# Performance work log

Measured on AMD Instinct MI355X. Metric: run time of the kernel, lower is better.

Reference implementation:

```python
import jax, jax.numpy as jnp
import numpy as np

EPS = 1e-5

def setup_inputs() -> dict:
    key = jax.random.key(0)
    ks = jax.random.split(key, 16)
    N, E, F_IN, DIM, C, G = 100000, 3200000, 128, 64, 10, 512
    inp = {}
    inp['x'] = jax.random.normal(ks[0], (N, F_IN), dtype=jnp.float32)
    inp['edge_index'] = jax.random.randint(ks[1], (2, E), 0, N, dtype=jnp.int64)
    inp['batch'] = jnp.sort(jax.random.randint(ks[2], (N,), 0, G, dtype=jnp.int64))
    inp['num_graphs'] = G
    def lin(k, fi, fo):
        s = 1.0 / np.sqrt(fi)
        kw, kb = jax.random.split(k)
        return (jax.random.uniform(kw, (fi, fo), jnp.float32, -s, s),
                jax.random.uniform(kb, (fo,), jnp.float32, -s, s))
    inp['W1'], inp['b1'] = lin(ks[3], F_IN, DIM)
    inp['W2'], inp['b2'] = lin(ks[4], DIM, DIM)
    inp['W3'], inp['b3'] = lin(ks[5], DIM, DIM)
    inp['W4'], inp['b4'] = lin(ks[6], DIM, DIM)
    for i in range(1, 5):
        inp[f'g{i}'] = jnp.ones((DIM,), jnp.float32)
        inp[f'be{i}'] = jnp.zeros((DIM,), jnp.float32)
    inp['fcW'], inp['fcb'] = lin(ks[7], DIM, C)
    return inp

def _bn(x, g, b):
    # training-mode BatchNorm1d: biased batch stats over node axis
    m = jnp.mean(x, axis=0)
    v = jnp.mean(jnp.square(x - m), axis=0)
    return g * (x - m) * jax.lax.rsqrt(v + EPS) + b

def _gcn_conv(x, W, b, row, col, norm, N):
    xl = x @ W                                  # [N, dim] dense transform first
    msg = norm[:, None] * xl[row]               # gather from source nodes
    out = jnp.zeros((N, xl.shape[1]), xl.dtype).at[col].add(msg)  # scatter to targets
    return out + b

def _forward(x, edge_index, batch, num_graphs,
             W1, b1, g1, be1, W2, b2, g2, be2,
             W3, b3, g3, be3, W4, b4, g4, be4, fcW, fcb):
    N = x.shape[0]
    loops = jnp.arange(N, dtype=edge_index.dtype)
    row = jnp.concatenate([edge_index[0], loops])   # sources (with self-loops)
    col = jnp.concatenate([edge_index[1], loops])   # targets
    deg = jnp.zeros((N,), x.dtype).at[col].add(1.0)
    dis = jnp.where(deg > 0, jax.lax.rsqrt(jnp.maximum(deg, 1.0)), 0.0)
    norm = dis[row] * dis[col]                      # symmetric GCN normalization
    h = _bn(jax.nn.relu(_gcn_conv(x, W1, b1, row, col, norm, N)), g1, be1)
    h = _bn(jax.nn.relu(_gcn_conv(h, W2, b2, row, col, norm, N)), g2, be2)
    h = _bn(jax.nn.relu(_gcn_conv(h, W3, b3, row, col, norm, N)), g3, be3)
    h = _bn(jax.nn.relu(_gcn_conv(h, W4, b4, row, col, norm, N)), g4, be4)
    # global mean pool over graphs
    sums = jax.ops.segment_sum(h, batch, num_segments=num_graphs)
    cnts = jax.ops.segment_sum(jnp.ones((N,), h.dtype), batch, num_segments=num_graphs)
    pooled = sums / jnp.maximum(cnts, 1.0)[:, None]
    logits = pooled @ fcW + fcb
    return jax.nn.log_softmax(logits, axis=-1)

def reference(x, edge_index, batch, num_graphs,
              W1, b1, g1, be1, W2, b2, g2, be2,
              W3, b3, g3, be3, W4, b4, g4, be4, fcW, fcb):
    return _forward(x, edge_index, batch, num_graphs,
                    W1, b1, g1, be1, W2, b2, g2, be2,
                    W3, b3, g3, be3, W4, b4, g4, be4, fcW, fcb)
```

## Files before the change

### kernel.cpp

```cpp
#include <hip/hip_runtime.h>
#include <hip/hip_bf16.h>
#include <math.h>

#define DIM 64
#define NBK_MAX 512
#define PCHUNK 4096
typedef _Float16 f16;
typedef unsigned int uint32;

__global__ __launch_bounds__(256) void k_hist(const int* __restrict__ col, int* __restrict__ bkcnt,
                                              int E, int nbk) {
  __shared__ int lc[NBK_MAX];
  int tid = threadIdx.x;
  for (int i = tid; i < nbk; i += 256) lc[i] = 0;
  __syncthreads();
  int b0 = blockIdx.x * PCHUNK;
  int b1 = min(E, b0 + PCHUNK);
  for (int e = b0 + tid; e < b1; e += 256) atomicAdd(&lc[col[e] >> 8], 1);
  __syncthreads();
  for (int i = tid; i < nbk; i += 256) { int c = lc[i]; if (c) atomicAdd(&bkcnt[i], c); }
}

__global__ __launch_bounds__(256) void k_scank(const int* __restrict__ cnt, int* __restrict__ offs,
                                               int* __restrict__ cur, int nbk) {
  __shared__ int ps[256];
  int t = threadIdx.x;
  int per = (nbk + 255) >> 8;
  int b0 = t * per;
  int s = 0;
  for (int i = 0; i < per; ++i) { int idx = b0 + i; if (idx < nbk) s += cnt[idx]; }
  ps[t] = s;
  __syncthreads();
  for (int d = 1; d < 256; d <<= 1) {
    int v = (t >= d) ? ps[t - d] : 0;
    __syncthreads();
    if (t >= d) ps[t] += v;
    __syncthreads();
  }
  int run = ps[t] - s;
  for (int i = 0; i < per; ++i) {
    int idx = b0 + i;
    if (idx < nbk) { offs[idx] = run; cur[idx] = run; run += cnt[idx]; }
  }
  if (t == 255) offs[nbk] = run;
}

__global__ __launch_bounds__(256) void k_part(const int* __restrict__ row, const int* __restrict__ col,
                                              int* __restrict__ bcur, uint32* __restrict__ recs,
                                              int E, int nbk) {
  __shared__ int lc[NBK_MAX];
  __shared__ int gb[NBK_MAX];
  int tid = threadIdx.x;
  for (int i = tid; i < nbk; i += 256) lc[i] = 0;
  __syncthreads();
  int b0 = blockIdx.x * PCHUNK;
  int b1 = min(E, b0 + PCHUNK);
  for (int e = b0 + tid; e < b1; e += 256) atomicAdd(&lc[col[e] >> 8], 1);
  __syncthreads();
  for (int i = tid; i < nbk; i += 256) {
    int c = lc[i];
    if (c) { gb[i] = atomicAdd(&bcur[i], c); lc[i] = 0; }
  }
  __syncthreads();
  for (int e = b0 + tid; e < b1; e += 256) {
    int r = row[e], c = col[e];
    int k = c >> 8;
    int pos = gb[k] + atomicAdd(&lc[k], 1);
    recs[pos] = ((uint32)r << 8) | (uint32)(c & 255);
  }
}

__global__ __launch_bounds__(256) void k_sort2(const uint32* __restrict__ recs, const int* __restrict__ keyoffs,
                                               int* __restrict__ csrs, int* __restrict__ offs,
                                               int* __restrict__ cnt, float* __restrict__ dis, int N) {
  __shared__ int lc[256];
  __shared__ int ps[256];
  __shared__ int pos[256];
  int b = blockIdx.x, tid = threadIdx.x;
  lc[tid] = 0;
  __syncthreads();
  int beg = keyoffs[b], end = keyoffs[b + 1];
  for (int p = beg + tid; p < end; p += 256) atomicAdd(&lc[recs[p] & 255], 1);
  __syncthreads();
  int my = lc[tid];
  ps[tid] = my;
  __syncthreads();
  for (int d = 1; d < 256; d <<= 1) {
    int v = (tid >= d) ? ps[tid - d] : 0;
    __syncthreads();
    if (tid >= d) ps[tid] += v;
    __syncthreads();
  }
  int epf = ps[tid] - my;
  pos[tid] = beg + epf;
  int node = (b << 8) + tid;
  if (node < N) {
    offs[node] = beg + epf;
    cnt[node] = my;
    dis[node] = rsqrtf((float)(my + 1));
  }
  __syncthreads();
  for (int p = beg + tid; p < end; p += 256) {
    uint32 r = recs[p];
    int q = atomicAdd(&pos[r & 255], 1);
    csrs[q] = (int)(r >> 8);
  }
}

__global__ __launch_bounds__(256) void k_gemm_in(const float* __restrict__ x, const float* __restrict__ W,
                                                 const float* __restrict__ dis, f16* __restrict__ xl,
                                                 int N, int FIN) {
  __shared__ float Ws[128 * DIM];
  __shared__ float vbuf[4][128];
  int tid = threadIdx.x;
  for (int i = tid; i < FIN * DIM; i += 256) Ws[i] = W[i];
  __syncthreads();
  int wave = tid >> 6, lane = tid & 63;
  int stride = gridDim.x * 4;
  for (int n = blockIdx.x * 4 + wave; n < N; n += stride) {
    const float* xr = x + (size_t)n * FIN;
    for (int k = lane; k < FIN; k += 64) vbuf[wave][k] = xr[k];
    float acc = 0.f;
#pragma unroll 16
    for (int k = 0; k < FIN; ++k) acc = fmaf(vbuf[wave][k], Ws[k * DIM + lane], acc);
    xl[(size_t)n * DIM + lane] = (f16)(acc * dis[n]);
  }
}

__global__ __launch_bounds__(256) void k_gemm_bn(const float* __restrict__ y, const float* __restrict__ W,
                                                 const float* __restrict__ gam, const float* __restrict__ bet,
                                                 const float* __restrict__ s1, const float* __restrict__ s2,
                                                 const float* __restrict__ dis, f16* __restrict__ xl, int N) {
  __shared__ float Ws[DIM * DIM];
  __shared__ float aL[DIM], cL[DIM];
  __shared__ float vbuf[4][DIM];
  int tid = threadIdx.x;
  for (int i = tid; i < DIM * DIM; i += 256) Ws[i] = W[i];
  if (tid < DIM) {
    float invN = 1.0f / (float)N;
    float m = s1[tid] * invN;
    float var = s2[tid] * invN - m * m;
    float inv = rsqrtf(var + 1e-5f);
    float a = gam[tid] * inv;
    aL[tid] = a;
    cL[tid] = fmaf(-m, a, bet[tid]);
  }
  __syncthreads();
  int wave = tid >> 6, lane = tid & 63;
  int stride = gridDim.x * 4;
  for (int n = blockIdx.x * 4 + wave; n < N; n += stride) {
    vbuf[wave][lane] = fmaf(aL[lane], y[(size_t)n * DIM + lane], cL[lane]);
    float acc = 0.f;
#pragma unroll
    for (int k = 0; k < DIM; ++k) acc = fmaf(vbuf[wave][k], Ws[k * DIM + lane], acc);
    xl[(size_t)n * DIM + lane] = (f16)(acc * dis[n]);
  }
}

__global__ __launch_bounds__(256) void k_agg(const f16* __restrict__ xl, const int* __restrict__ offs,
                                             const int* __restrict__ cnt, const int* __restrict__ src,
                                             const float* __restrict__ dis, const float* __restrict__ bias,
                                             float* __restrict__ y, float* __restrict__ s1,
                                             float* __restrict__ s2, int N) {
  int tid = threadIdx.x;
  int wave = tid >> 6, lane = tid & 63;
  float ls = 0.f, lq = 0.f;
  float b = bias[lane];
  int stride = gridDim.x * 4;
  for (int n = blockIdx.x * 4 + wave; n < N; n += stride) {
    float di = dis[n];
    float acc = (float)xl[((size_t)n << 6) + lane];
    int p = offs[n];
    int end = p + cnt[n];
    for (; p + 7 < end; p += 8) {
      int a0 = src[p],     a1 = src[p + 1], a2 = src[p + 2], a3 = src[p + 3];
      int a4 = src[p + 4], a5 = src[p + 5], a6 = src[p + 6], a7 = src[p + 7];
      float v0 = (float)xl[((size_t)a0 << 6) + lane];
      float v1 = (float)xl[((size_t)a1 << 6) + lane];
      float v2 = (float)xl[((size_t)a2 << 6) + lane];
      float v3 = (float)xl[((size_t)a3 << 6) + lane];
      float v4 = (float)xl[((size_t)a4 << 6) + lane];
      float v5 = (float)xl[((size_t)a5 << 6) + lane];
      float v6 = (float)xl[((size_t)a6 << 6) + lane];
      float v7 = (float)xl[((size_t)a7 << 6) + lane];
      acc += ((v0 + v1) + (v2 + v3)) + ((v4 + v5) + (v6 + v7));
    }
    for (; p < end; ++p) acc += (float)xl[((size_t)src[p] << 6) + lane];
    float yv = fmaxf(fmaf(di, acc, b), 0.f);
    y[((size_t)n << 6) + lane] = yv;
    ls += yv;
    lq = fmaf(yv, yv, lq);
  }
  __shared__ float rbuf[256];
  rbuf[tid] = ls;
  __syncthreads();
  if (tid < 64) atomicAdd(&s1[tid], rbuf[tid] + rbuf[tid + 64] + rbuf[tid + 128] + rbuf[tid + 192]);
  __syncthreads();
  rbuf[tid] = lq;
  __syncthreads();
  if (tid < 64) atomicAdd(&s2[tid], rbuf[tid] + rbuf[tid + 64] + rbuf[tid + 128] + rbuf[tid + 192]);
}

__global__ __launch_bounds__(256) void k_pool(const float* __restrict__ y, const float* __restrict__ gam,
                                              const float* __restrict__ bet, const float* __restrict__ s1,
                                              const float* __restrict__ s2, const int* __restrict__ batch,
                                              float* __restrict__ pooled, float* __restrict__ gcnt,
                                              int N, int chunk) {
  __shared__ float aL[DIM], cL[DIM];
  int tid = threadIdx.x;
  if (tid < DIM) {
    float invN = 1.0f / (float)N;
    float m = s1[tid] * invN;
    float var = s2[tid] * invN - m * m;
    float inv = rsqrtf(var + 1e-5f);
    float a = gam[tid] * inv;
    aL[tid] = a;
    cL[tid] = fmaf(-m, a, bet[tid]);
  }
  __syncthreads();
  int wave = tid >> 6, lane = tid & 63;
  int wid = blockIdx.x * 4 + wave;
  int n0 = wid * chunk;
  int n1 = min(N, n0 + chunk);
  if (n0 >= N) return;
  int cur_g = batch[n0];
  float acc = 0.f;
  int cntn = 0;
  for (int n = n0; n < n1; ++n) {
    int gi = batch[n];
    if (gi != cur_g) {
      atomicAdd(&pooled[(size_t)cur_g * DIM + lane], acc);
      if (lane == 0) atomicAdd(&gcnt[cur_g], (float)cntn);
      cur_g = gi; acc = 0.f; cntn = 0;
    }
    acc += fmaf(aL[lane], y[(size_t)n * DIM + lane], cL[lane]);
    ++cntn;
  }
  atomicAdd(&pooled[(size_t)cur_g * DIM + lane], acc);
  if (lane == 0) atomicAdd(&gcnt[cur_g], (float)cntn);
}

__global__ __launch_bounds__(256) void k_head(const float* __restrict__ pooled, const float* __restrict__ gcnt,
                                              const float* __restrict__ fcW, const float* __restrict__ fcb,
                                              float* __restrict__ out, int G, int C) {
  int g = blockIdx.x * 256 + threadIdx.x;
  if (g >= G) return;
  float z[16];
  for (int c = 0; c < C; ++c) z[c] = fcb[c];
  float inv = 1.f / fmaxf(gcnt[g], 1.f);
  for (int f = 0; f < DIM; ++f) {
    float p = pooled[(size_t)g * DIM + f] * inv;
    for (int c = 0; c < C; ++c) z[c] = fmaf(p, fcW[f * C + c], z[c]);
  }
  float m = -1e30f;
  for (int c = 0; c < C; ++c) m = fmaxf(m, z[c]);
  float s = 0.f;
  for (int c = 0; c < C; ++c) s += expf(z[c] - m);
  float ls = logf(s);
  for (int c = 0; c < C; ++c) out[(size_t)g * C + c] = z[c] - m - ls;
}

extern "C" void kernel_launch(void* const* d_in, const int* in_sizes, int n_in,
                              void* d_out, int out_size, void* d_ws, size_t ws_size,
                              hipStream_t stream) {
  const float* x    = (const float*)d_in[0];
  const int*   ei   = (const int*)d_in[1];
  const int*   batch= (const int*)d_in[2];
  const float* W1 = (const float*)d_in[4];
  const float* b1 = (const float*)d_in[5];
  const float* W2 = (const float*)d_in[6];
  const float* b2 = (const float*)d_in[7];
  const float* W3 = (const float*)d_in[8];
  const float* b3 = (const float*)d_in[9];
  const float* W4 = (const float*)d_in[10];
  const float* b4 = (const float*)d_in[11];
  const float* g1 = (const float*)d_in[12];
  const float* be1= (const float*)d_in[13];
  const float* g2 = (const float*)d_in[14];
  const float* be2= (const float*)d_in[15];
  const float* g3 = (const float*)d_in[16];
  const float* be3= (const float*)d_in[17];
  const float* g4 = (const float*)d_in[18];
  const float* be4= (const float*)d_in[19];
  const float* fcW= (const float*)d_in[20];
  const float* fcb= (const float*)d_in[21];
  float* out = (float*)d_out;

  int N   = in_sizes[2];
  int E   = in_sizes[1] / 2;
  int FIN = in_sizes[4] / DIM;
  int C   = in_sizes[21];
  int G   = out_size / C;

  int nbk = (N + 255) >> 8;

  char* ws = (char*)d_ws;
  size_t off = 0;
  auto alloc = [&](size_t bytes) { size_t o = off; off = (off + bytes + 255) & ~(size_t)255; return o; };
  size_t o_bkc  = alloc((size_t)nbk * 4);
  size_t o_bn   = alloc(4 * 2 * 64 * 4);
  size_t o_pool = alloc((size_t)G * DIM * 4);
  size_t o_gcnt = alloc((size_t)G * 4);
  size_t zero_bytes = off;
  size_t o_ko   = alloc((size_t)(nbk + 1) * 4);
  size_t o_cur  = alloc((size_t)nbk * 4);
  size_t o_offs = alloc((size_t)N * 4);
  size_t o_cnt  = alloc((size_t)N * 4);
  size_t o_dis  = alloc((size_t)N * 4);
  size_t o_recs = alloc((size_t)E * 4);
  size_t o_csr  = alloc((size_t)E * 4);
  size_t o_xl   = alloc((size_t)N * DIM * 2);
  size_t o_y    = alloc((size_t)N * DIM * 4);
  (void)ws_size;

  int*    bkcnt  = (int*)(ws + o_bkc);
  float*  bn     = (float*)(ws + o_bn);
  float*  pooled = (float*)(ws + o_pool);
  float*  gcnt   = (float*)(ws + o_gcnt);
  int*    keyoffs= (int*)(ws + o_ko);
  int*    bcur   = (int*)(ws + o_cur);
  int*    offs   = (int*)(ws + o_offs);
  int*    cnt    = (int*)(ws + o_cnt);
  float*  dis    = (float*)(ws + o_dis);
  uint32* recs   = (uint32*)(ws + o_recs);
  int*    csrs   = (int*)(ws + o_csr);
  f16*    xl     = (f16*)(ws + o_xl);
  float*  y      = (float*)(ws + o_y);

  hipMemsetAsync(d_ws, 0, zero_bytes, stream);

  const int* row  = ei;
  const int* colp = ei + E;
  int pblk = (E + PCHUNK - 1) / PCHUNK;

  k_hist<<<pblk, 256, 0, stream>>>(colp, bkcnt, E, nbk);
  k_scank<<<1, 256, 0, stream>>>(bkcnt, keyoffs, bcur, nbk);
  k_part<<<pblk, 256, 0, stream>>>(row, colp, bcur, recs, E, nbk);
  k_sort2<<<nbk, 256, 0, stream>>>(recs, keyoffs, csrs, offs, cnt, dis, N);

  k_gemm_in<<<1024, 256, 0, stream>>>(x, W1, dis, xl, N, FIN);
  k_agg<<<2048, 256, 0, stream>>>(xl, offs, cnt, csrs, dis, b1, y, bn + 0, bn + 64, N);
  k_gemm_bn<<<2048, 256, 0, stream>>>(y, W2, g1, be1, bn + 0, bn + 64, dis, xl, N);
  k_agg<<<2048, 256, 0, stream>>>(xl, offs, cnt, csrs, dis, b2, y, bn + 128, bn + 192, N);
  k_gemm_bn<<<2048, 256, 0, stream>>>(y, W3, g2, be2, bn + 128, bn + 192, dis, xl, N);
  k_agg<<<2048, 256, 0, stream>>>(xl, offs, cnt, csrs, dis, b3, y, bn + 256, bn + 320, N);
  k_gemm_bn<<<2048, 256, 0, stream>>>(y, W4, g3, be3, bn + 256, bn + 320, dis, xl, N);
  k_agg<<<2048, 256, 0, stream>>>(xl, offs, cnt, csrs, dis, b4, y, bn + 384, bn + 448, N);
  int nwaves = 2048;
  int chunk = (N + nwaves - 1) / nwaves;
  k_pool<<<nwaves / 4, 256, 0, stream>>>(y, g4, be4, bn + 384, bn + 448, batch, pooled, gcnt, N, chunk);
  k_head<<<(G + 255) / 256, 256, 0, stream>>>(pooled, gcnt, fcW, fcb, out, G, C);
}
```

Baseline: 998.4 us.

## Register-resident GEMM weights with readlane broadcast, fold BN into weights, fp16 activations

The GEMM kernels now keep each lane's weight column in registers and broadcast the row values with readlane, which removes the LDS staging and its syncs. The BatchNorm scale is folded into the weights and the shift into a constant bias per column. The intermediate activation y is stored as fp16 instead of fp32, halving its write and read traffic. The aggregation unroll grows to 16 and the 32-bit index math replaces size_t. The trade-offs are high VGPR pressure (128 floats for the first GEMM), lower occupancy, and reduced precision of the stored activations.

```diff
diff --git a/kernel.cpp b/kernel.cpp
--- a/kernel.cpp
+++ b/kernel.cpp
@@ -7,6 +7,10 @@
 #define PCHUNK 4096
 typedef _Float16 f16;
 typedef unsigned int uint32;
+
+__device__ __forceinline__ float bcast(float v, int k) {
+  return __uint_as_float(__builtin_amdgcn_readlane(__float_as_uint(v), k));
+}
 
 __global__ __launch_bounds__(256) void k_hist(const int* __restrict__ col, int* __restrict__ bkcnt,
                                               int E, int nbk) {
@@ -108,36 +112,100 @@
 }
 
 __global__ __launch_bounds__(256) void k_gemm_in(const float* __restrict__ x, const float* __restrict__ W,
-                                                 const float* __restrict__ dis, f16* __restrict__ xl,
-                                                 int N, int FIN) {
-  __shared__ float Ws[128 * DIM];
-  __shared__ float vbuf[4][128];
-  int tid = threadIdx.x;
-  for (int i = tid; i < FIN * DIM; i += 256) Ws[i] = W[i];
-  __syncthreads();
-  int wave = tid >> 6, lane = tid & 63;
+                                                 const float* __restrict__ dis, f16* __restrict__ xl, int N) {
+  int tid = threadIdx.x;
+  int lane = tid & 63, wave = tid >> 6;
+  float w[128];
+#pragma unroll
+  for (int k = 0; k < 128; ++k) w[k] = W[k * DIM + lane];
   int stride = gridDim.x * 4;
   for (int n = blockIdx.x * 4 + wave; n < N; n += stride) {
-    const float* xr = x + (size_t)n * FIN;
-    for (int k = lane; k < FIN; k += 64) vbuf[wave][k] = xr[k];
+    const float* xr = x + (size_t)n * 128;
+    float x0 = xr[lane];
+    float x1 = xr[64 + lane];
     float acc = 0.f;
-#pragma unroll 16
-    for (int k = 0; k < FIN; ++k) acc = fmaf(vbuf[wave][k], Ws[k * DIM + lane], acc);
-    xl[(size_t)n * DIM + lane] = (f16)(acc * dis[n]);
-  }
-}
-
-__global__ __launch_bounds__(256) void k_gemm_bn(const float* __restrict__ y, const float* __restrict__ W,
+#pragma unroll
+    for (int k = 0; k < 64; ++k) acc = fmaf(bcast(x0, k), w[k], acc);
+#pragma unroll
+    for (int k = 0; k < 64; ++k) acc = fmaf(bcast(x1, k), w[64 + k], acc);
+    xl[((uint32)n << 6) | lane] = (f16)(acc * dis[n]);
+  }
+}
+
+__global__ __launch_bounds__(256) void k_gemm_bn(const f16* __restrict__ y16, const float* __restrict__ W,
                                                  const float* __restrict__ gam, const float* __restrict__ bet,
                                                  const float* __restrict__ s1, const float* __restrict__ s2,
-                                                 const float* __restrict__ dis, f16* __restrict__ xl, int N) {
-  __shared__ float Ws[DIM * DIM];
+                                                 const float* __restrict__ dis, f16* __restrict__ xl,
+                                                 int N, float invN) {
+  int tid = threadIdx.x;
+  int lane = tid & 63, wave = tid >> 6;
+  float w[64];
+  float cb = 0.f;
+#pragma unroll
+  for (int k = 0; k < 64; ++k) {
+    float m = s1[k] * invN;
+    float var = s2[k] * invN - m * m;
+    float a = gam[k] * rsqrtf(var + 1e-5f);
+    float c = fmaf(-m, a, bet[k]);
+    float wk = W[k * DIM + lane];
+    w[k] = a * wk;
+    cb = fmaf(c, wk, cb);
+  }
+  int stride = gridDim.x * 4;
+  for (int n = blockIdx.x * 4 + wave; n < N; n += stride) {
+    float yv = (float)y16[((uint32)n << 6) | lane];
+    float acc = cb;
+#pragma unroll
+    for (int k = 0; k < 64; ++k) acc = fmaf(bcast(yv, k), w[k], acc);
+    xl[((uint32)n << 6) | lane] = (f16)(acc * dis[n]);
+  }
+}
+
+__global__ __launch_bounds__(256) void k_agg(const f16* __restrict__ xl, const int* __restrict__ offs,
+                                             const int* __restrict__ cnt, const int* __restrict__ src,
+                                             const float* __restrict__ dis, const float* __restrict__ bias,
+                                             f16* __restrict__ y, float* __restrict__ s1,
+                                             float* __restrict__ s2, int N) {
+  int tid = threadIdx.x;
+  int wave = tid >> 6, lane = tid & 63;
+  float ls = 0.f, lq = 0.f;
+  float b = bias[lane];
+  int stride = gridDim.x * 4;
+  for (int n = blockIdx.x * 4 + wave; n < N; n += stride) {
+    float di = dis[n];
+    float acc = (float)xl[((uint32)n << 6) | lane];
+    int p = offs[n];
+    int end = p + cnt[n];
+    for (; p + 15 < end; p += 16) {
+      float s = 0.f;
+#pragma unroll
+      for (int j = 0; j < 16; ++j) s += (float)xl[((uint32)src[p + j] << 6) | lane];
+      acc += s;
+    }
+    for (; p < end; ++p) acc += (float)xl[((uint32)src[p] << 6) | lane];
+    float yv = fmaxf(fmaf(di, acc, b), 0.f);
+    y[((uint32)n << 6) | lane] = (f16)yv;
+    ls += yv;
+    lq = fmaf(yv, yv, lq);
+  }
+  __shared__ float rbuf[256];
+  rbuf[tid] = ls;
+  __syncthreads();
+  if (tid < 64) atomicAdd(&s1[tid], rbuf[tid] + rbuf[tid + 64] + rbuf[tid + 128] + rbuf[tid + 192]);
+  __syncthreads();
+  rbuf[tid] = lq;
+  __syncthreads();
+  if (tid < 64) atomicAdd(&s2[tid], rbuf[tid] + rbuf[tid + 64] + rbuf[tid + 128] + rbuf[tid + 192]);
+}
+
+__global__ __launch_bounds__(256) void k_pool(const f16* __restrict__ y, const float* __restrict__ gam,
+                                              const float* __restrict__ bet, const float* __restrict__ s1,
+                                              const float* __restrict__ s2, const int* __restrict__ batch,
+                                              float* __restrict__ pooled, float* __restrict__ gcnt,
+                                              int N, int chunk, float invN) {
   __shared__ float aL[DIM], cL[DIM];
-  __shared__ float vbuf[4][DIM];
-  int tid = threadIdx.x;
-  for (int i = tid; i < DIM * DIM; i += 256) Ws[i] = W[i];
+  int tid = threadIdx.x;
   if (tid < DIM) {
-    float invN = 1.0f / (float)N;
     float m = s1[tid] * invN;
     float var = s2[tid] * invN - m * m;
     float inv = rsqrtf(var + 1e-5f);
@@ -147,82 +215,11 @@
   }
   __syncthreads();
   int wave = tid >> 6, lane = tid & 63;
-  int stride = gridDim.x * 4;
-  for (int n = blockIdx.x * 4 + wave; n < N; n += stride) {
-    vbuf[wave][lane] = fmaf(aL[lane], y[(size_t)n * DIM + lane], cL[lane]);
-    float acc = 0.f;
-#pragma unroll
-    for (int k = 0; k < DIM; ++k) acc = fmaf(vbuf[wave][k], Ws[k * DIM + lane], acc);
-    xl[(size_t)n * DIM + lane] = (f16)(acc * dis[n]);
-  }
-}
-
-__global__ __launch_bounds__(256) void k_agg(const f16* __restrict__ xl, const int* __restrict__ offs,
-                                             const int* __restrict__ cnt, const int* __restrict__ src,
-                                             const float* __restrict__ dis, const float* __restrict__ bias,
-                                             float* __restrict__ y, float* __restrict__ s1,
-                                             float* __restrict__ s2, int N) {
-  int tid = threadIdx.x;
-  int wave = tid >> 6, lane = tid & 63;
-  float ls = 0.f, lq = 0.f;
-  float b = bias[lane];
-  int stride = gridDim.x * 4;
-  for (int n = blockIdx.x * 4 + wave; n < N; n += stride) {
-    float di = dis[n];
-    float acc = (float)xl[((size_t)n << 6) + lane];
-    int p = offs[n];
-    int end = p + cnt[n];
-    for (; p + 7 < end; p += 8) {
-      int a0 = src[p],     a1 = src[p + 1], a2 = src[p + 2], a3 = src[p + 3];
-      int a4 = src[p + 4], a5 = src[p + 5], a6 = src[p + 6], a7 = src[p + 7];
-      float v0 = (float)xl[((size_t)a0 << 6) + lane];
-      float v1 = (float)xl[((size_t)a1 << 6) + lane];
-      float v2 = (float)xl[((size_t)a2 << 6) + lane];
-      float v3 = (float)xl[((size_t)a3 << 6) + lane];
-      float v4 = (float)xl[((size_t)a4 << 6) + lane];
-      float v5 = (float)xl[((size_t)a5 << 6) + lane];
-      float v6 = (float)xl[((size_t)a6 << 6) + lane];
-      float v7 = (float)xl[((size_t)a7 << 6) + lane];
-      acc += ((v0 + v1) + (v2 + v3)) + ((v4 + v5) + (v6 + v7));
-    }
-    for (; p < end; ++p) acc += (float)xl[((size_t)src[p] << 6) + lane];
-    float yv = fmaxf(fmaf(di, acc, b), 0.f);
-    y[((size_t)n << 6) + lane] = yv;
-    ls += yv;
-    lq = fmaf(yv, yv, lq);
-  }
-  __shared__ float rbuf[256];
-  rbuf[tid] = ls;
-  __syncthreads();
-  if (tid < 64) atomicAdd(&s1[tid], rbuf[tid] + rbuf[tid + 64] + rbuf[tid + 128] + rbuf[tid + 192]);
-  __syncthreads();
-  rbuf[tid] = lq;
-  __syncthreads();
-  if (tid < 64) atomicAdd(&s2[tid], rbuf[tid] + rbuf[tid + 64] + rbuf[tid + 128] + rbuf[tid + 192]);
-}
-
-__global__ __launch_bounds__(256) void k_pool(const float* __restrict__ y, const float* __restrict__ gam,
-                                              const float* __restrict__ bet, const float* __restrict__ s1,
-                                              const float* __restrict__ s2, const int* __restrict__ batch,
-                                              float* __restrict__ pooled, float* __restrict__ gcnt,
-                                              int N, int chunk) {
-  __shared__ float aL[DIM], cL[DIM];
-  int tid = threadIdx.x;
-  if (tid < DIM) {
-    float invN = 1.0f / (float)N;
-    float m = s1[tid] * invN;
-    float var = s2[tid] * invN - m * m;
-    float inv = rsqrtf(var + 1e-5f);
-    float a = gam[tid] * inv;
-    aL[tid] = a;
-    cL[tid] = fmaf(-m, a, bet[tid]);
-  }
-  __syncthreads();
-  int wave = tid >> 6, lane = tid & 63;
   int wid = blockIdx.x * 4 + wave;
   int n0 = wid * chunk;
   int n1 = min(N, n0 + chunk);
   if (n0 >= N) return;
+  float aV = aL[lane], cV = cL[lane];
   int cur_g = batch[n0];
   float acc = 0.f;
   int cntn = 0;
@@ -233,7 +230,7 @@
       if (lane == 0) atomicAdd(&gcnt[cur_g], (float)cntn);
       cur_g = gi; acc = 0.f; cntn = 0;
     }
-    acc += fmaf(aL[lane], y[(size_t)n * DIM + lane], cL[lane]);
+    acc += fmaf(aV, (float)y[((uint32)n << 6) | lane], cV);
     ++cntn;
   }
   atomicAdd(&pooled[(size_t)cur_g * DIM + lane], acc);
@@ -288,9 +285,9 @@
 
   int N   = in_sizes[2];
   int E   = in_sizes[1] / 2;
-  int FIN = in_sizes[4] / DIM;
   int C   = in_sizes[21];
   int G   = out_size / C;
+  float invN = 1.0f / (float)N;
 
   int nbk = (N + 255) >> 8;
 
@@ -310,7 +307,7 @@
   size_t o_recs = alloc((size_t)E * 4);
   size_t o_csr  = alloc((size_t)E * 4);
   size_t o_xl   = alloc((size_t)N * DIM * 2);
-  size_t o_y    = alloc((size_t)N * DIM * 4);
+  size_t o_y    = alloc((size_t)N * DIM * 2);
   (void)ws_size;
 
   int*    bkcnt  = (int*)(ws + o_bkc);
@@ -325,7 +322,7 @@
   uint32* recs   = (uint32*)(ws + o_recs);
   int*    csrs   = (int*)(ws + o_csr);
   f16*    xl     = (f16*)(ws + o_xl);
-  float*  y      = (float*)(ws + o_y);
+  f16*    y      = (f16*)(ws + o_y);
 
   hipMemsetAsync(d_ws, 0, zero_bytes, stream);
 
@@ -338,16 +335,16 @@
   k_part<<<pblk, 256, 0, stream>>>(row, colp, bcur, recs, E, nbk);
   k_sort2<<<nbk, 256, 0, stream>>>(recs, keyoffs, csrs, offs, cnt, dis, N);
 
-  k_gemm_in<<<1024, 256, 0, stream>>>(x, W1, dis, xl, N, FIN);
+  k_gemm_in<<<2048, 256, 0, stream>>>(x, W1, dis, xl, N);
   k_agg<<<2048, 256, 0, stream>>>(xl, offs, cnt, csrs, dis, b1, y, bn + 0, bn + 64, N);
-  k_gemm_bn<<<2048, 256, 0, stream>>>(y, W2, g1, be1, bn + 0, bn + 64, dis, xl, N);
+  k_gemm_bn<<<2048, 256, 0, stream>>>(y, W2, g1, be1, bn + 0, bn + 64, dis, xl, N, invN);
   k_agg<<<2048, 256, 0, stream>>>(xl, offs, cnt, csrs, dis, b2, y, bn + 128, bn + 192, N);
-  k_gemm_bn<<<2048, 256, 0, stream>>>(y, W3, g2, be2, bn + 128, bn + 192, dis, xl, N);
+  k_gemm_bn<<<2048, 256, 0, stream>>>(y, W3, g2, be2, bn + 128, bn + 192, dis, xl, N, invN);
   k_agg<<<2048, 256, 0, stream>>>(xl, offs, cnt, csrs, dis, b3, y, bn + 256, bn + 320, N);
-  k_gemm_bn<<<2048, 256, 0, stream>>>(y, W4, g3, be3, bn + 256, bn + 320, dis, xl, N);
+  k_gemm_bn<<<2048, 256, 0, stream>>>(y, W4, g3, be3, bn + 256, bn + 320, dis, xl, N, invN);
   k_agg<<<2048, 256, 0, stream>>>(xl, offs, cnt, csrs, dis, b4, y, bn + 384, bn + 448, N);
   int nwaves = 2048;
   int chunk = (N + nwaves - 1) / nwaves;
-  k_pool<<<nwaves / 4, 256, 0, stream>>>(y, g4, be4, bn + 384, bn + 448, batch, pooled, gcnt, N, chunk);
+  k_pool<<<nwaves / 4, 256, 0, stream>>>(y, g4, be4, bn + 384, bn + 448, batch, pooled, gcnt, N, chunk, invN);
   k_head<<<(G + 255) / 256, 256, 0, stream>>>(pooled, gcnt, fcW, fcb, out, G, C);
 }
```

After: 1.039 ms. +4.1%, slower.
